# Optimization experiments

Measured on AMD Instinct MI355X. Metric: run time of the kernel, lower is better.

Reference implementation:

```python
import jax, jax.numpy as jnp
import numpy as np


def setup_inputs() -> dict:
    key = jax.random.key(0)
    ks = jax.random.split(key, 8)
    B, L, D, H, Dh = 2, 2048, 1024, 16, 64
    scale = 1.0 / np.sqrt(D)
    return {
        "inputs_q": jax.random.normal(ks[0], (B, L, D), jnp.float32),
        "inputs_kv": jax.random.normal(ks[1], (B, L, D), jnp.float32),
        "mask_k": jax.random.uniform(ks[2], (B, L), jnp.float32),
        "Wq": jax.random.normal(ks[3], (D, H, Dh), jnp.float32) * scale,
        "bq": jnp.zeros((H, Dh), jnp.float32),
        "Wk": jax.random.normal(ks[4], (D, H, Dh), jnp.float32) * scale,
        "bk": jnp.zeros((H, Dh), jnp.float32),
        "Wv": jax.random.normal(ks[5], (D, H, Dh), jnp.float32) * scale,
        "bv": jnp.zeros((H, Dh), jnp.float32),
        "Wo": jax.random.normal(ks[6], (H, Dh, D), jnp.float32) * (1.0 / np.sqrt(D)),
        "bo": jnp.zeros((D,), jnp.float32),
    }


def reference(inputs_q, inputs_kv, mask_k, Wq, bq, Wk, bk, Wv, bv, Wo, bo):
    # QKV projections: [B,L,D] x [D,H,Dh] -> [B,L,H,Dh]
    q = jnp.einsum("bld,dhk->blhk", inputs_q, Wq) + bq
    k = jnp.einsum("bld,dhk->blhk", inputs_kv, Wk) + bk
    v = jnp.einsum("bld,dhk->blhk", inputs_kv, Wv) + bv
    # vector mask applied to values per key position
    v = mask_k[:, :, None, None] * v
    head_dim = q.shape[-1]
    q = q / jnp.sqrt(jnp.asarray(head_dim, q.dtype))
    # attention scores [B,H,Lq,Lk]
    scores = jnp.einsum("bqhk,bshk->bhqs", q, k)
    probs = jax.nn.softmax(scores, axis=-1)
    # weighted values [B,Lq,H,Dh]
    x = jnp.einsum("bhqs,bshk->bqhk", probs, v)
    # output projection over (head, head_dim)
    out = jnp.einsum("bqhk,hkd->bqd", x, Wo) + bo
    return out
```

## Files before the change

### kernel.cpp

```cpp
#include <hip/hip_runtime.h>
#include <stdint.h>

typedef __attribute__((ext_vector_type(8))) short bf16x8;
typedef __attribute__((ext_vector_type(4))) float f32x4;
typedef __attribute__((ext_vector_type(16))) float f32x16;
typedef __attribute__((ext_vector_type(4))) unsigned short us4;
typedef __attribute__((ext_vector_type(4))) unsigned int u32x4;

#define AS1 __attribute__((address_space(1)))
#define AS3 __attribute__((address_space(3)))

static constexpr int Lq = 2048;
static constexpr int Dm = 1024;
static constexpr int NH = 16;
static constexpr int DH = 64;

__device__ __forceinline__ unsigned short f2bf(float x) {
  union { float f; uint32_t u; } v; v.f = x;
  uint32_t r = v.u + 0x7FFFu + ((v.u >> 16) & 1u);
  return (unsigned short)(r >> 16);
}

#if __has_builtin(__builtin_amdgcn_exp2f)
__device__ __forceinline__ float exp2_fast(float x) { return __builtin_amdgcn_exp2f(x); }
#else
__device__ __forceinline__ float exp2_fast(float x) {
  float r; asm volatile("v_exp_f32 %0, %1" : "=v"(r) : "v"(x)); return r;
}
#endif

__device__ __forceinline__ uint32_t cvtpk_bf16(float lo, float hi) {
  uint32_t r;
  asm("v_cvt_pk_bf16_f32 %0, %1, %2" : "=v"(r) : "v"(lo), "v"(hi));
  return r;
}

__device__ __forceinline__ f32x16 zero16() {
  f32x16 z;
#pragma unroll
  for (int i = 0; i < 16; ++i) z[i] = 0.f;
  return z;
}

__global__ __launch_bounds__(256) void cvt2_kernel(
    const float* __restrict__ s0, const float* __restrict__ s1,
    unsigned short* __restrict__ d0, unsigned short* __restrict__ d1, int n4) {
  const float* src = blockIdx.y ? s1 : s0;
  unsigned short* dst = blockIdx.y ? d1 : d0;
  int idx = blockIdx.x * 256 + threadIdx.x;
  int stride = gridDim.x * 256;
  for (int i = idx; i < n4; i += stride) {
    float4 f = ((const float4*)src)[i];
    us4 o = { f2bf(f.x), f2bf(f.y), f2bf(f.z), f2bf(f.w) };
    ((us4*)dst)[i] = o;
  }
}

__global__ __launch_bounds__(256) void tpose_kernel(
    const float* __restrict__ W0, const float* __restrict__ W1,
    const float* __restrict__ W2, const float* __restrict__ W3,
    unsigned short* __restrict__ T0, unsigned short* __restrict__ T1,
    unsigned short* __restrict__ T2, unsigned short* __restrict__ T3) {
  __shared__ float tile[32][33];
  const float* src; unsigned short* dst;
  switch (blockIdx.z) {
    case 0: src = W0; dst = T0; break;
    case 1: src = W1; dst = T1; break;
    case 2: src = W2; dst = T2; break;
    default: src = W3; dst = T3; break;
  }
  int x = threadIdx.x & 31, ys = threadIdx.x >> 5;
  int bx = blockIdx.x * 32, by = blockIdx.y * 32;
  for (int i = 0; i < 4; ++i) {
    int y = ys * 4 + i;
    tile[y][x] = src[(size_t)(by + y) * Dm + bx + x];
  }
  __syncthreads();
  for (int i = 0; i < 4; ++i) {
    int y = ys * 4 + i;
    dst[(size_t)(bx + y) * Dm + by + x] = f2bf(tile[x][y]);
  }
}

__global__ __launch_bounds__(512) void gemm_kernel(
    const unsigned short* __restrict__ A0, const unsigned short* __restrict__ A1,
    const unsigned short* __restrict__ W0, const unsigned short* __restrict__ W1,
    const unsigned short* __restrict__ W2,
    const float* __restrict__ b0, const float* __restrict__ b1,
    const float* __restrict__ b2, const float* __restrict__ mask,
    unsigned short* __restrict__ Qw, unsigned short* __restrict__ Kw,
    unsigned short* __restrict__ Vtw, float* __restrict__ Of, int modeBase) {
  const int mode = modeBase + blockIdx.z;
  const unsigned short* Ap = (mode == 1 || mode == 2) ? A1 : A0;
  const unsigned short* Wp = (mode == 1) ? W1 : ((mode == 2) ? W2 : W0);
  const float* bias = (mode == 1) ? b1 : ((mode == 2) ? b2 : b0);

  const int tid = threadIdx.x, lane = tid & 63, wid = tid >> 6;
  const int wm = wid >> 1, wn = wid & 1;
  const int m0 = blockIdx.x * 128, n0 = blockIdx.y * 128;
  const int ln = lane & 15, kg = lane >> 4;

  __shared__ __align__(16) unsigned short smem[24576];

  f32x4 acc[2][4];
#pragma unroll
  for (int i = 0; i < 2; ++i)
#pragma unroll
    for (int j = 0; j < 4; ++j) acc[i][j] = f32x4{0.f, 0.f, 0.f, 0.f};

  const int srow = tid >> 2;
  const int schx = (tid & 3) ^ ((srow >> 1) & 3);
  auto stage_g = [&](int buf, int k0) {
    __builtin_amdgcn_global_load_lds(
        (const AS1 unsigned int*)(Ap + (size_t)(m0 + srow) * Dm + k0 + schx * 8),
        (AS3 unsigned int*)&smem[buf * 4096 + wid * 512], 16, 0, 0);
    __builtin_amdgcn_global_load_lds(
        (const AS1 unsigned int*)(Wp + (size_t)(n0 + srow) * Dm + k0 + schx * 8),
        (AS3 unsigned int*)&smem[12288 + buf * 4096 + wid * 512], 16, 0, 0);
  };
  auto comp_g = [&](int buf) {
    const unsigned short* As = &smem[buf * 4096];
    const unsigned short* Bs = &smem[12288 + buf * 4096];
    const int rsw = kg ^ ((ln >> 1) & 3);
    bf16x8 af[2], bfv[4];
#pragma unroll
    for (int f = 0; f < 2; ++f)
      af[f] = *(const bf16x8*)&As[(wm * 32 + f * 16 + ln) * 32 + rsw * 8];
#pragma unroll
    for (int f = 0; f < 4; ++f)
      bfv[f] = *(const bf16x8*)&Bs[(wn * 64 + f * 16 + ln) * 32 + rsw * 8];
    __builtin_amdgcn_s_setprio(1);
#pragma unroll
    for (int mf = 0; mf < 2; ++mf)
#pragma unroll
      for (int nf = 0; nf < 4; ++nf)
        acc[mf][nf] = __builtin_amdgcn_mfma_f32_16x16x32_bf16(af[mf], bfv[nf],
                                                              acc[mf][nf], 0, 0, 0);
    __builtin_amdgcn_s_setprio(0);
  };

  stage_g(0, 0);
  stage_g(1, 32);
  for (int tt = 0; tt < 30; tt += 3) {
#pragma unroll
    for (int j = 0; j < 3; ++j) {
      const int t = tt + j;
      asm volatile("s_waitcnt vmcnt(2)" ::: "memory");
      asm volatile("s_barrier" ::: "memory");
      if (t < 30) stage_g((j + 2) % 3, (t + 2) * 32);
      comp_g(j);
    }
  }
  asm volatile("s_waitcnt vmcnt(2)" ::: "memory");
  asm volatile("s_barrier" ::: "memory");
  comp_g(0);
  asm volatile("s_waitcnt vmcnt(0)" ::: "memory");
  asm volatile("s_barrier" ::: "memory");
  comp_g(1);

  __syncthreads();
  unsigned short* ep = smem + wid * 2560;
  const int rowbase = m0 + wm * 32;
  const int colbase = n0 + wn * 64;

  if (mode <= 1) {
    unsigned short* dstbase = (mode == 0) ? Qw : Kw;
    const int hh = colbase >> 6;
    const int bb_ = rowbase >> 11, lb = rowbase & 2047;
    unsigned short* dst = dstbase + ((size_t)(bb_ * NH + hh) * Lq + lb) * DH;
    const float sc = (mode == 0) ? 0.18033688f : 1.0f;
    for (int nf = 0; nf < 4; ++nf) {
      const float bv_ = bias[colbase + nf * 16 + ln];
      for (int mf = 0; mf < 2; ++mf)
        for (int r = 0; r < 4; ++r)
          ep[(mf * 16 + kg * 4 + r) * 72 + nf * 16 + ln] =
              f2bf((acc[mf][nf][r] + bv_) * sc);
    }
    for (int it = 0; it < 4; ++it) {
      const int e = it * 64 + lane;
      const int rr = e >> 3, c = (e & 7) * 8;
      *(bf16x8*)(dst + (size_t)rr * DH + c) = *(const bf16x8*)&ep[rr * 72 + c];
    }
  } else if (mode == 2) {
    const int hh = colbase >> 6;
    const int bb_ = rowbase >> 11;
    const int l0 = rowbase & 2047;
    unsigned short* dst = Vtw + (size_t)(bb_ * NH + hh) * DH * Lq;
    for (int nf = 0; nf < 4; ++nf) {
      const int dh2 = nf * 16 + ln;
      const float bv_ = bias[colbase + dh2];
      for (int mf = 0; mf < 2; ++mf)
        for (int r = 0; r < 4; ++r) {
          const int rl = mf * 16 + kg * 4 + r;
          ep[dh2 * 40 + rl] = f2bf((acc[mf][nf][r] + bv_) * mask[rowbase + rl]);
        }
    }
    for (int it = 0; it < 4; ++it) {
      const int e = it * 64 + lane;
      const int dr = e >> 2, c = (e & 3) * 8;
      *(bf16x8*)(dst + (size_t)dr * Lq + l0 + c) = *(const bf16x8*)&ep[dr * 40 + c];
    }
  } else {
    float* epf = (float*)smem + wid * 1280;
    for (int mf = 0; mf < 2; ++mf) {
      for (int nf = 0; nf < 4; ++nf) {
        const float bv_ = bias[colbase + nf * 16 + ln];
        for (int r = 0; r < 4; ++r)
          epf[(kg * 4 + r) * 68 + nf * 16 + ln] = acc[mf][nf][r] + bv_;
      }
      for (int it = 0; it < 4; ++it) {
        const int e = it * 64 + lane;
        const int rr = e >> 4, c = (lane & 15) * 4;
        *(f32x4*)(Of + (size_t)(rowbase + mf * 16 + rr) * Dm + colbase + c) =
            *(const f32x4*)&epf[rr * 68 + c];
      }
    }
  }
}

__global__ __launch_bounds__(512) void attn_kernel(
    const unsigned short* __restrict__ Q, const unsigned short* __restrict__ K,
    const unsigned short* __restrict__ Vt, unsigned short* __restrict__ X) {
  const int tid = threadIdx.x, lane = tid & 63, wv = tid >> 6;
  const int lq = lane & 31, hi = lane >> 5;
  const int wq = wv & 3, half = wv >> 2;
  const int h = blockIdx.y, b = blockIdx.z;
  const int q0 = blockIdx.x * 128 + wq * 32;

  const size_t bh = (size_t)b * NH + h;
  const unsigned short* Qp = Q + bh * Lq * DH;
  const unsigned short* Kp = K + bh * Lq * DH + (size_t)half * 1024 * DH;
  const unsigned short* Vp = Vt + bh * DH * Lq + half * 1024;

  __shared__ __align__(16) unsigned short smem[24576];
  unsigned short* Klds = smem + half * 12288;
  unsigned short* Vlds = smem + half * 12288 + 6144;

  const int st = tid & 255;
  const int kr = st >> 3, kc = st & 7;
  const unsigned short* ksrc = Kp + (size_t)kr * DH + ((kc ^ (kr & 7)) * 8);
  const int vr = st >> 2, vc = st & 3;
  const unsigned short* vsrc = Vp + (size_t)vr * Lq + ((vc ^ ((vr >> 1) & 3)) * 8);

  auto stage = [&](int buf, const unsigned short* kp, const unsigned short* vp) {
    __builtin_amdgcn_global_load_lds((const AS1 unsigned int*)kp,
        (AS3 unsigned int*)&Klds[buf * 2048 + wq * 512], 16, 0, 0);
    __builtin_amdgcn_global_load_lds((const AS1 unsigned int*)vp,
        (AS3 unsigned int*)&Vlds[buf * 2048 + wq * 512], 16, 0, 0);
  };

  bf16x8 qf[4];
#pragma unroll
  for (int ks = 0; ks < 4; ++ks)
    qf[ks] = *(const bf16x8*)(Qp + (size_t)(q0 + lq) * DH + ks * 16 + hi * 8);

  bf16x8 onesf;
#pragma unroll
  for (int i = 0; i < 8; ++i) onesf[i] = (short)0x3F80;

  f32x16 o0 = zero16(), o1 = zero16(), lacc = zero16();

  auto compute = [&](const unsigned short* Kb, const unsigned short* Vb) {
    f32x16 s = zero16();
    __builtin_amdgcn_s_setprio(1);
#pragma unroll
    for (int ks = 0; ks < 4; ++ks) {
      const bf16x8 kfr =
          *(const bf16x8*)&Kb[lq * 64 + (((2 * ks + hi) ^ (lq & 7)) * 8)];
      s = __builtin_amdgcn_mfma_f32_32x32x16_bf16(kfr, qf[ks], s, 0, 0, 0);
    }
    __builtin_amdgcn_s_setprio(0);

    float p[16];
#pragma unroll
    for (int i = 0; i < 16; ++i) p[i] = exp2_fast(s[i]);

    uint32_t a00 = cvtpk_bf16(p[0],  p[1]),  a01 = cvtpk_bf16(p[2],  p[3]);
    uint32_t a10 = cvtpk_bf16(p[4],  p[5]),  a11 = cvtpk_bf16(p[6],  p[7]);
    uint32_t a20 = cvtpk_bf16(p[8],  p[9]),  a21 = cvtpk_bf16(p[10], p[11]);
    uint32_t a30 = cvtpk_bf16(p[12], p[13]), a31 = cvtpk_bf16(p[14], p[15]);
    asm volatile("v_permlane32_swap_b32 %0, %1" : "+v"(a00), "+v"(a10));
    asm volatile("v_permlane32_swap_b32 %0, %1" : "+v"(a01), "+v"(a11));
    asm volatile("v_permlane32_swap_b32 %0, %1" : "+v"(a20), "+v"(a30));
    asm volatile("v_permlane32_swap_b32 %0, %1" : "+v"(a21), "+v"(a31));
    u32x4 pw0 = {a00, a01, a10, a11};
    u32x4 pw1 = {a20, a21, a30, a31};
    const bf16x8 pa0 = *(const bf16x8*)&pw0;
    const bf16x8 pa1 = *(const bf16x8*)&pw1;

    __builtin_amdgcn_s_setprio(1);
    lacc = __builtin_amdgcn_mfma_f32_32x32x16_bf16(pa0, onesf, lacc, 0, 0, 0);
    lacc = __builtin_amdgcn_mfma_f32_32x32x16_bf16(pa1, onesf, lacc, 0, 0, 0);
    {
      const int sw0 = (lq >> 1) & 3;
      const bf16x8 vb0 = *(const bf16x8*)&Vb[lq * 32 + ((hi ^ sw0) * 8)];
      const bf16x8 vb1 = *(const bf16x8*)&Vb[lq * 32 + (((2 + hi) ^ sw0) * 8)];
      o0 = __builtin_amdgcn_mfma_f32_32x32x16_bf16(pa0, vb0, o0, 0, 0, 0);
      o0 = __builtin_amdgcn_mfma_f32_32x32x16_bf16(pa1, vb1, o0, 0, 0, 0);
      const int dh1 = 32 + lq;
      const int sw1 = (dh1 >> 1) & 3;
      const bf16x8 vb2 = *(const bf16x8*)&Vb[dh1 * 32 + ((hi ^ sw1) * 8)];
      const bf16x8 vb3 = *(const bf16x8*)&Vb[dh1 * 32 + (((2 + hi) ^ sw1) * 8)];
      o1 = __builtin_amdgcn_mfma_f32_32x32x16_bf16(pa0, vb2, o1, 0, 0, 0);
      o1 = __builtin_amdgcn_mfma_f32_32x32x16_bf16(pa1, vb3, o1, 0, 0, 0);
    }
    __builtin_amdgcn_s_setprio(0);
  };

  stage(0, ksrc, vsrc);
  stage(1, ksrc + 2048, vsrc + 32);
  const unsigned short* kpre = ksrc + 4096;
  const unsigned short* vpre = vsrc + 64;
  for (int tt = 0; tt < 30; tt += 3) {
#pragma unroll
    for (int j = 0; j < 3; ++j) {
      asm volatile("s_waitcnt vmcnt(2)" ::: "memory");
      asm volatile("s_barrier" ::: "memory");
      stage((j + 2) % 3, kpre, vpre);
      kpre += 2048; vpre += 32;
      compute(&Klds[j * 2048], &Vlds[j * 2048]);
    }
  }
  asm volatile("s_waitcnt vmcnt(2)" ::: "memory");
  asm volatile("s_barrier" ::: "memory");
  compute(&Klds[0], &Vlds[0]);
  asm volatile("s_waitcnt vmcnt(0)" ::: "memory");
  asm volatile("s_barrier" ::: "memory");
  compute(&Klds[2048], &Vlds[2048]);

  __syncthreads();
  float* cs = (float*)smem;
  float* po = cs + wq * 2048;
  float* pl = cs + 8192 + wq * 32;
  if (half == 1) {
#pragma unroll
    for (int r = 0; r < 16; ++r) {
      const int qrow = (r & 3) + 8 * (r >> 2) + 4 * hi;
      po[qrow * 64 + lq]      = o0[r];
      po[qrow * 64 + 32 + lq] = o1[r];
    }
    if (lq == 0) {
#pragma unroll
      for (int r = 0; r < 16; ++r)
        pl[(r & 3) + 8 * (r >> 2) + 4 * hi] = lacc[r];
    }
  }
  __syncthreads();
  if (half == 0) {
    unsigned short ou0[16], ou1[16];
#pragma unroll
    for (int r = 0; r < 16; ++r) {
      const int qrow = (r & 3) + 8 * (r >> 2) + 4 * hi;
      const float iv = 1.0f / (lacc[r] + pl[qrow]);
      ou0[r] = f2bf((o0[r] + po[qrow * 64 + lq]) * iv);
      ou1[r] = f2bf((o1[r] + po[qrow * 64 + 32 + lq]) * iv);
    }
    unsigned short* ep = (unsigned short*)po;
#pragma unroll
    for (int r = 0; r < 16; ++r) {
      const int qrow = (r & 3) + 8 * (r >> 2) + 4 * hi;
      ep[qrow * 72 + lq]      = ou0[r];
      ep[qrow * 72 + 32 + lq] = ou1[r];
    }
#pragma unroll
    for (int it = 0; it < 4; ++it) {
      const int e = it * 64 + lane;
      const int row = e >> 3, ch = e & 7;
      *(bf16x8*)(X + (size_t)(b * Lq + q0 + row) * Dm + h * DH + ch * 8) =
          *(const bf16x8*)&ep[row * 72 + ch * 8];
    }
  }
}

extern "C" void kernel_launch(void* const* d_in, const int* in_sizes, int n_in,
                              void* d_out, int out_size, void* d_ws, size_t ws_size,
                              hipStream_t stream) {
  (void)in_sizes; (void)n_in; (void)out_size; (void)ws_size;
  const float* inputs_q  = (const float*)d_in[0];
  const float* inputs_kv = (const float*)d_in[1];
  const float* mask_k    = (const float*)d_in[2];
  const float* Wq = (const float*)d_in[3];
  const float* bq = (const float*)d_in[4];
  const float* Wk = (const float*)d_in[5];
  const float* bk = (const float*)d_in[6];
  const float* Wv = (const float*)d_in[7];
  const float* bv = (const float*)d_in[8];
  const float* Wo = (const float*)d_in[9];
  const float* bo = (const float*)d_in[10];
  float* out = (float*)d_out;

  unsigned short* ws = (unsigned short*)d_ws;
  const size_t BIG = 4194304;
  const size_t WSZ = 1048576;
  unsigned short* Xq  = ws;
  unsigned short* Xkv = Xq + BIG;
  unsigned short* Wqt = Xkv + BIG;
  unsigned short* Wkt = Wqt + WSZ;
  unsigned short* Wvt = Wkt + WSZ;
  unsigned short* Wot = Wvt + WSZ;
  unsigned short* Qw  = Wot + WSZ;
  unsigned short* Kw  = Qw + BIG;
  unsigned short* Vtw = Kw + BIG;
  unsigned short* Xat = Vtw + BIG;

  cvt2_kernel<<<dim3(512, 2), 256, 0, stream>>>(inputs_q, inputs_kv, Xq, Xkv,
                                                (int)(BIG / 4));
  tpose_kernel<<<dim3(32, 32, 4), 256, 0, stream>>>(Wq, Wk, Wv, Wo, Wqt, Wkt, Wvt, Wot);
  gemm_kernel<<<dim3(32, 8, 3), 512, 0, stream>>>(Xq, Xkv, Wqt, Wkt, Wvt, bq, bk, bv,
                                                  mask_k, Qw, Kw, Vtw, nullptr, 0);
  attn_kernel<<<dim3(16, 16, 2), 512, 0, stream>>>(Qw, Kw, Vtw, Xat);
  gemm_kernel<<<dim3(32, 8, 1), 512, 0, stream>>>(Xat, nullptr, Wot, nullptr, nullptr,
                                                  bo, nullptr, nullptr, nullptr,
                                                  nullptr, nullptr, nullptr, out, 3);
}
```

Baseline: 104.6 us.

## Split attention keys across four wave groups with double-buffered LDS and XCD-aware block mapping

The attention kernel grows from 512 to 1024 threads per block, so four wave groups each process a quarter of the key sequence instead of two halves. The key loop changes from a three-buffer prefetch ring to a two-buffer scheme with an extra barrier after each compute step. Partial outputs are reduced serially through LDS in three rounds. A flattened 1D grid remaps block IDs so that blocks of the same batch and head land on the same XCD for L2 reuse. The aim is more split-K parallelism and better cache locality, at the cost of more barriers, less prefetch depth and a longer reduction epilogue.

```diff
diff --git a/kernel.cpp b/kernel.cpp
--- a/kernel.cpp
+++ b/kernel.cpp
@@ -218,23 +218,27 @@
   }
 }
 
-__global__ __launch_bounds__(512) void attn_kernel(
+__global__ __launch_bounds__(1024) void attn_kernel(
     const unsigned short* __restrict__ Q, const unsigned short* __restrict__ K,
     const unsigned short* __restrict__ Vt, unsigned short* __restrict__ X) {
   const int tid = threadIdx.x, lane = tid & 63, wv = tid >> 6;
   const int lq = lane & 31, hi = lane >> 5;
-  const int wq = wv & 3, half = wv >> 2;
-  const int h = blockIdx.y, b = blockIdx.z;
-  const int q0 = blockIdx.x * 128 + wq * 32;
+  const int wq = wv & 3, qu = wv >> 2;
+  const int bid = blockIdx.x;
+  const int slot = bid >> 3;
+  const int g = (bid & 7) * 4 + (slot >> 4);
+  const int qt = slot & 15;
+  const int h = g & 15, b = g >> 4;
+  const int q0 = qt * 128 + wq * 32;
 
   const size_t bh = (size_t)b * NH + h;
   const unsigned short* Qp = Q + bh * Lq * DH;
-  const unsigned short* Kp = K + bh * Lq * DH + (size_t)half * 1024 * DH;
-  const unsigned short* Vp = Vt + bh * DH * Lq + half * 1024;
-
-  __shared__ __align__(16) unsigned short smem[24576];
-  unsigned short* Klds = smem + half * 12288;
-  unsigned short* Vlds = smem + half * 12288 + 6144;
+  const unsigned short* Kp = K + bh * Lq * DH + (size_t)qu * 512 * DH;
+  const unsigned short* Vp = Vt + bh * DH * Lq + qu * 512;
+
+  __shared__ __align__(16) unsigned short smem[32768];
+  unsigned short* Klds = smem + qu * 8192;
+  unsigned short* Vlds = smem + qu * 8192 + 4096;
 
   const int st = tid & 255;
   const int kr = st >> 3, kc = st & 7;
@@ -260,7 +264,9 @@
 
   f32x16 o0 = zero16(), o1 = zero16(), lacc = zero16();
 
-  auto compute = [&](const unsigned short* Kb, const unsigned short* Vb) {
+  auto compute = [&](int buf) {
+    const unsigned short* Kb = &Klds[buf * 2048];
+    const unsigned short* Vb = &Vlds[buf * 2048];
     f32x16 s = zero16();
     __builtin_amdgcn_s_setprio(1);
 #pragma unroll
@@ -311,56 +317,63 @@
   stage(1, ksrc + 2048, vsrc + 32);
   const unsigned short* kpre = ksrc + 4096;
   const unsigned short* vpre = vsrc + 64;
-  for (int tt = 0; tt < 30; tt += 3) {
-#pragma unroll
-    for (int j = 0; j < 3; ++j) {
-      asm volatile("s_waitcnt vmcnt(2)" ::: "memory");
-      asm volatile("s_barrier" ::: "memory");
-      stage((j + 2) % 3, kpre, vpre);
-      kpre += 2048; vpre += 32;
-      compute(&Klds[j * 2048], &Vlds[j * 2048]);
-    }
+#pragma unroll 2
+  for (int t = 0; t < 14; ++t) {
+    asm volatile("s_waitcnt vmcnt(2)" ::: "memory");
+    asm volatile("s_barrier" ::: "memory");
+    compute(t & 1);
+    asm volatile("s_waitcnt lgkmcnt(0)" ::: "memory");
+    asm volatile("s_barrier" ::: "memory");
+    stage(t & 1, kpre, vpre);
+    kpre += 2048; vpre += 32;
   }
   asm volatile("s_waitcnt vmcnt(2)" ::: "memory");
   asm volatile("s_barrier" ::: "memory");
-  compute(&Klds[0], &Vlds[0]);
+  compute(0);
   asm volatile("s_waitcnt vmcnt(0)" ::: "memory");
   asm volatile("s_barrier" ::: "memory");
-  compute(&Klds[2048], &Vlds[2048]);
+  compute(1);
 
   __syncthreads();
   float* cs = (float*)smem;
   float* po = cs + wq * 2048;
   float* pl = cs + 8192 + wq * 32;
-  if (half == 1) {
+#pragma unroll
+  for (int rr = 1; rr < 4; ++rr) {
+    if (qu == rr) {
+#pragma unroll
+      for (int r = 0; r < 16; ++r) {
+        const int qrow = (r & 3) + 8 * (r >> 2) + 4 * hi;
+        po[qrow * 64 + lq]      = o0[r];
+        po[qrow * 64 + 32 + lq] = o1[r];
+      }
+      if (lq == 0) {
+#pragma unroll
+        for (int r = 0; r < 16; ++r)
+          pl[(r & 3) + 8 * (r >> 2) + 4 * hi] = lacc[r];
+      }
+    }
+    __syncthreads();
+    if (qu == 0) {
+#pragma unroll
+      for (int r = 0; r < 16; ++r) {
+        const int qrow = (r & 3) + 8 * (r >> 2) + 4 * hi;
+        o0[r]   += po[qrow * 64 + lq];
+        o1[r]   += po[qrow * 64 + 32 + lq];
+        lacc[r] += pl[qrow];
+      }
+    }
+    __syncthreads();
+  }
+
+  if (qu == 0) {
+    unsigned short* ep = (unsigned short*)po;
 #pragma unroll
     for (int r = 0; r < 16; ++r) {
       const int qrow = (r & 3) + 8 * (r >> 2) + 4 * hi;
-      po[qrow * 64 + lq]      = o0[r];
-      po[qrow * 64 + 32 + lq] = o1[r];
-    }
-    if (lq == 0) {
-#pragma unroll
-      for (int r = 0; r < 16; ++r)
-        pl[(r & 3) + 8 * (r >> 2) + 4 * hi] = lacc[r];
-    }
-  }
-  __syncthreads();
-  if (half == 0) {
-    unsigned short ou0[16], ou1[16];
-#pragma unroll
-    for (int r = 0; r < 16; ++r) {
-      const int qrow = (r & 3) + 8 * (r >> 2) + 4 * hi;
-      const float iv = 1.0f / (lacc[r] + pl[qrow]);
-      ou0[r] = f2bf((o0[r] + po[qrow * 64 + lq]) * iv);
-      ou1[r] = f2bf((o1[r] + po[qrow * 64 + 32 + lq]) * iv);
-    }
-    unsigned short* ep = (unsigned short*)po;
-#pragma unroll
-    for (int r = 0; r < 16; ++r) {
-      const int qrow = (r & 3) + 8 * (r >> 2) + 4 * hi;
-      ep[qrow * 72 + lq]      = ou0[r];
-      ep[qrow * 72 + 32 + lq] = ou1[r];
+      const float iv = 1.0f / lacc[r];
+      ep[qrow * 72 + lq]      = f2bf(o0[r] * iv);
+      ep[qrow * 72 + 32 + lq] = f2bf(o1[r] * iv);
     }
 #pragma unroll
     for (int it = 0; it < 4; ++it) {
@@ -408,7 +421,7 @@
   tpose_kernel<<<dim3(32, 32, 4), 256, 0, stream>>>(Wq, Wk, Wv, Wo, Wqt, Wkt, Wvt, Wot);
   gemm_kernel<<<dim3(32, 8, 3), 512, 0, stream>>>(Xq, Xkv, Wqt, Wkt, Wvt, bq, bk, bv,
                                                   mask_k, Qw, Kw, Vtw, nullptr, 0);
-  attn_kernel<<<dim3(16, 16, 2), 512, 0, stream>>>(Qw, Kw, Vtw, Xat);
+  attn_kernel<<<dim3(512, 1, 1), 1024, 0, stream>>>(Qw, Kw, Vtw, Xat);
   gemm_kernel<<<dim3(32, 8, 1), 512, 0, stream>>>(Xat, nullptr, Wot, nullptr, nullptr,
                                                   bo, nullptr, nullptr, nullptr,
                                                   nullptr, nullptr, nullptr, out, 3);
```

Measured after the change: 108.1 us. 1.03x slower.

## Give each attention wave two 32-row query tiles and remap blocks across XCDs

Applied to the files above, without the earlier changes.

The attention kernel drops from 8 waves to 4 per block. Each wave now handles 64 query rows as two 32-row MFMA tiles, so every K/V fragment read from LDS feeds twice as many MFMAs. Each thread issues four global-to-LDS loads per stage instead of two, with the vmcnt waits adjusted to match. The launch grid becomes 1D with a block-index remap that groups (batch, head) pairs per XCD for L2 locality, at the cost of roughly doubled accumulator registers per wave.

```diff
diff --git a/kernel.cpp b/kernel.cpp
--- a/kernel.cpp
+++ b/kernel.cpp
@@ -218,14 +218,18 @@
   }
 }
 
-__global__ __launch_bounds__(512) void attn_kernel(
+__global__ __launch_bounds__(256) void attn_kernel(
     const unsigned short* __restrict__ Q, const unsigned short* __restrict__ K,
     const unsigned short* __restrict__ Vt, unsigned short* __restrict__ X) {
   const int tid = threadIdx.x, lane = tid & 63, wv = tid >> 6;
   const int lq = lane & 31, hi = lane >> 5;
-  const int wq = wv & 3, half = wv >> 2;
-  const int h = blockIdx.y, b = blockIdx.z;
-  const int q0 = blockIdx.x * 128 + wq * 32;
+  const int qw = wv & 1, half = wv >> 1;
+  const int bid = blockIdx.x;
+  const int slot = bid >> 3;
+  const int g = (bid & 7) * 4 + (slot >> 4);
+  const int qt = slot & 15;
+  const int h = g & 15, b = g >> 4;
+  const int q0 = qt * 128 + qw * 64;
 
   const size_t bh = (size_t)b * NH + h;
   const unsigned short* Qp = Q + bh * Lq * DH;
@@ -236,134 +240,166 @@
   unsigned short* Klds = smem + half * 12288;
   unsigned short* Vlds = smem + half * 12288 + 6144;
 
-  const int st = tid & 255;
-  const int kr = st >> 3, kc = st & 7;
-  const unsigned short* ksrc = Kp + (size_t)kr * DH + ((kc ^ (kr & 7)) * 8);
-  const int vr = st >> 2, vc = st & 3;
-  const unsigned short* vsrc = Vp + (size_t)vr * Lq + ((vc ^ ((vr >> 1) & 3)) * 8);
-
-  auto stage = [&](int buf, const unsigned short* kp, const unsigned short* vp) {
-    __builtin_amdgcn_global_load_lds((const AS1 unsigned int*)kp,
-        (AS3 unsigned int*)&Klds[buf * 2048 + wq * 512], 16, 0, 0);
-    __builtin_amdgcn_global_load_lds((const AS1 unsigned int*)vp,
-        (AS3 unsigned int*)&Vlds[buf * 2048 + wq * 512], 16, 0, 0);
+  const int kcA = qw * 64 + lane;
+  const int krow = kcA >> 3, kch = kcA & 7;
+  const unsigned short* ksrcA = Kp + (size_t)krow * DH + ((kch ^ (krow & 7)) * 8);
+  const int vrow = kcA >> 2, vch = kcA & 3;
+  const unsigned short* vsrcA = Vp + (size_t)vrow * Lq + ((vch ^ ((vrow >> 1) & 3)) * 8);
+
+  auto stage = [&](int buf, int koff, int voff) {
+    __builtin_amdgcn_global_load_lds((const AS1 unsigned int*)(ksrcA + koff),
+        (AS3 unsigned int*)&Klds[buf * 2048 + qw * 512], 16, 0, 0);
+    __builtin_amdgcn_global_load_lds((const AS1 unsigned int*)(ksrcA + 1024 + koff),
+        (AS3 unsigned int*)&Klds[buf * 2048 + 1024 + qw * 512], 16, 0, 0);
+    __builtin_amdgcn_global_load_lds((const AS1 unsigned int*)(vsrcA + voff),
+        (AS3 unsigned int*)&Vlds[buf * 2048 + qw * 512], 16, 0, 0);
+    __builtin_amdgcn_global_load_lds((const AS1 unsigned int*)(vsrcA + 32 * Lq + voff),
+        (AS3 unsigned int*)&Vlds[buf * 2048 + 1024 + qw * 512], 16, 0, 0);
   };
 
-  bf16x8 qf[4];
-#pragma unroll
-  for (int ks = 0; ks < 4; ++ks)
-    qf[ks] = *(const bf16x8*)(Qp + (size_t)(q0 + lq) * DH + ks * 16 + hi * 8);
+  bf16x8 qfA[4], qfB[4];
+#pragma unroll
+  for (int ks = 0; ks < 4; ++ks) {
+    qfA[ks] = *(const bf16x8*)(Qp + (size_t)(q0 + lq) * DH + ks * 16 + hi * 8);
+    qfB[ks] = *(const bf16x8*)(Qp + (size_t)(q0 + 32 + lq) * DH + ks * 16 + hi * 8);
+  }
 
   bf16x8 onesf;
 #pragma unroll
   for (int i = 0; i < 8; ++i) onesf[i] = (short)0x3F80;
 
-  f32x16 o0 = zero16(), o1 = zero16(), lacc = zero16();
-
-  auto compute = [&](const unsigned short* Kb, const unsigned short* Vb) {
-    f32x16 s = zero16();
+  f32x16 o0A = zero16(), o1A = zero16(), lA = zero16();
+  f32x16 o0B = zero16(), o1B = zero16(), lB = zero16();
+
+  auto compute = [&](int buf) {
+    const unsigned short* Kb = &Klds[buf * 2048];
+    const unsigned short* Vb = &Vlds[buf * 2048];
+    f32x16 sA = zero16(), sB = zero16();
     __builtin_amdgcn_s_setprio(1);
 #pragma unroll
     for (int ks = 0; ks < 4; ++ks) {
       const bf16x8 kfr =
           *(const bf16x8*)&Kb[lq * 64 + (((2 * ks + hi) ^ (lq & 7)) * 8)];
-      s = __builtin_amdgcn_mfma_f32_32x32x16_bf16(kfr, qf[ks], s, 0, 0, 0);
+      sA = __builtin_amdgcn_mfma_f32_32x32x16_bf16(kfr, qfA[ks], sA, 0, 0, 0);
+      sB = __builtin_amdgcn_mfma_f32_32x32x16_bf16(kfr, qfB[ks], sB, 0, 0, 0);
     }
     __builtin_amdgcn_s_setprio(0);
 
-    float p[16];
-#pragma unroll
-    for (int i = 0; i < 16; ++i) p[i] = exp2_fast(s[i]);
-
-    uint32_t a00 = cvtpk_bf16(p[0],  p[1]),  a01 = cvtpk_bf16(p[2],  p[3]);
-    uint32_t a10 = cvtpk_bf16(p[4],  p[5]),  a11 = cvtpk_bf16(p[6],  p[7]);
-    uint32_t a20 = cvtpk_bf16(p[8],  p[9]),  a21 = cvtpk_bf16(p[10], p[11]);
-    uint32_t a30 = cvtpk_bf16(p[12], p[13]), a31 = cvtpk_bf16(p[14], p[15]);
+    float pA[16], pB[16];
+#pragma unroll
+    for (int i = 0; i < 16; ++i) { pA[i] = exp2_fast(sA[i]); pB[i] = exp2_fast(sB[i]); }
+
+    uint32_t a00 = cvtpk_bf16(pA[0],  pA[1]),  a01 = cvtpk_bf16(pA[2],  pA[3]);
+    uint32_t a10 = cvtpk_bf16(pA[4],  pA[5]),  a11 = cvtpk_bf16(pA[6],  pA[7]);
+    uint32_t a20 = cvtpk_bf16(pA[8],  pA[9]),  a21 = cvtpk_bf16(pA[10], pA[11]);
+    uint32_t a30 = cvtpk_bf16(pA[12], pA[13]), a31 = cvtpk_bf16(pA[14], pA[15]);
     asm volatile("v_permlane32_swap_b32 %0, %1" : "+v"(a00), "+v"(a10));
     asm volatile("v_permlane32_swap_b32 %0, %1" : "+v"(a01), "+v"(a11));
     asm volatile("v_permlane32_swap_b32 %0, %1" : "+v"(a20), "+v"(a30));
     asm volatile("v_permlane32_swap_b32 %0, %1" : "+v"(a21), "+v"(a31));
-    u32x4 pw0 = {a00, a01, a10, a11};
-    u32x4 pw1 = {a20, a21, a30, a31};
-    const bf16x8 pa0 = *(const bf16x8*)&pw0;
-    const bf16x8 pa1 = *(const bf16x8*)&pw1;
+    uint32_t b00 = cvtpk_bf16(pB[0],  pB[1]),  b01 = cvtpk_bf16(pB[2],  pB[3]);
+    uint32_t b10 = cvtpk_bf16(pB[4],  pB[5]),  b11 = cvtpk_bf16(pB[6],  pB[7]);
+    uint32_t b20 = cvtpk_bf16(pB[8],  pB[9]),  b21 = cvtpk_bf16(pB[10], pB[11]);
+    uint32_t b30 = cvtpk_bf16(pB[12], pB[13]), b31 = cvtpk_bf16(pB[14], pB[15]);
+    asm volatile("v_permlane32_swap_b32 %0, %1" : "+v"(b00), "+v"(b10));
+    asm volatile("v_permlane32_swap_b32 %0, %1" : "+v"(b01), "+v"(b11));
+    asm volatile("v_permlane32_swap_b32 %0, %1" : "+v"(b20), "+v"(b30));
+    asm volatile("v_permlane32_swap_b32 %0, %1" : "+v"(b21), "+v"(b31));
+    u32x4 pwA0 = {a00, a01, a10, a11}, pwA1 = {a20, a21, a30, a31};
+    u32x4 pwB0 = {b00, b01, b10, b11}, pwB1 = {b20, b21, b30, b31};
+    const bf16x8 paA0 = *(const bf16x8*)&pwA0, paA1 = *(const bf16x8*)&pwA1;
+    const bf16x8 paB0 = *(const bf16x8*)&pwB0, paB1 = *(const bf16x8*)&pwB1;
 
     __builtin_amdgcn_s_setprio(1);
-    lacc = __builtin_amdgcn_mfma_f32_32x32x16_bf16(pa0, onesf, lacc, 0, 0, 0);
-    lacc = __builtin_amdgcn_mfma_f32_32x32x16_bf16(pa1, onesf, lacc, 0, 0, 0);
+    lA = __builtin_amdgcn_mfma_f32_32x32x16_bf16(paA0, onesf, lA, 0, 0, 0);
+    lA = __builtin_amdgcn_mfma_f32_32x32x16_bf16(paA1, onesf, lA, 0, 0, 0);
+    lB = __builtin_amdgcn_mfma_f32_32x32x16_bf16(paB0, onesf, lB, 0, 0, 0);
+    lB = __builtin_amdgcn_mfma_f32_32x32x16_bf16(paB1, onesf, lB, 0, 0, 0);
     {
       const int sw0 = (lq >> 1) & 3;
       const bf16x8 vb0 = *(const bf16x8*)&Vb[lq * 32 + ((hi ^ sw0) * 8)];
       const bf16x8 vb1 = *(const bf16x8*)&Vb[lq * 32 + (((2 + hi) ^ sw0) * 8)];
-      o0 = __builtin_amdgcn_mfma_f32_32x32x16_bf16(pa0, vb0, o0, 0, 0, 0);
-      o0 = __builtin_amdgcn_mfma_f32_32x32x16_bf16(pa1, vb1, o0, 0, 0, 0);
+      o0A = __builtin_amdgcn_mfma_f32_32x32x16_bf16(paA0, vb0, o0A, 0, 0, 0);
+      o0A = __builtin_amdgcn_mfma_f32_32x32x16_bf16(paA1, vb1, o0A, 0, 0, 0);
+      o0B = __builtin_amdgcn_mfma_f32_32x32x16_bf16(paB0, vb0, o0B, 0, 0, 0);
+      o0B = __builtin_amdgcn_mfma_f32_32x32x16_bf16(paB1, vb1, o0B, 0, 0, 0);
       const int dh1 = 32 + lq;
       const int sw1 = (dh1 >> 1) & 3;
       const bf16x8 vb2 = *(const bf16x8*)&Vb[dh1 * 32 + ((hi ^ sw1) * 8)];
       const bf16x8 vb3 = *(const bf16x8*)&Vb[dh1 * 32 + (((2 + hi) ^ sw1) * 8)];
-      o1 = __builtin_amdgcn_mfma_f32_32x32x16_bf16(pa0, vb2, o1, 0, 0, 0);
-      o1 = __builtin_amdgcn_mfma_f32_32x32x16_bf16(pa1, vb3, o1, 0, 0, 0);
+      o1A = __builtin_amdgcn_mfma_f32_32x32x16_bf16(paA0, vb2, o1A, 0, 0, 0);
+      o1A = __builtin_amdgcn_mfma_f32_32x32x16_bf16(paA1, vb3, o1A, 0, 0, 0);
+      o1B = __builtin_amdgcn_mfma_f32_32x32x16_bf16(paB0, vb2, o1B, 0, 0, 0);
+      o1B = __builtin_amdgcn_mfma_f32_32x32x16_bf16(paB1, vb3, o1B, 0, 0, 0);
     }
     __builtin_amdgcn_s_setprio(0);
   };
 
-  stage(0, ksrc, vsrc);
-  stage(1, ksrc + 2048, vsrc + 32);
-  const unsigned short* kpre = ksrc + 4096;
-  const unsigned short* vpre = vsrc + 64;
+  stage(0, 0, 0);
+  stage(1, 2048, 32);
   for (int tt = 0; tt < 30; tt += 3) {
 #pragma unroll
     for (int j = 0; j < 3; ++j) {
-      asm volatile("s_waitcnt vmcnt(2)" ::: "memory");
+      const int t = tt + j;
+      asm volatile("s_waitcnt vmcnt(4)" ::: "memory");
       asm volatile("s_barrier" ::: "memory");
-      stage((j + 2) % 3, kpre, vpre);
-      kpre += 2048; vpre += 32;
-      compute(&Klds[j * 2048], &Vlds[j * 2048]);
-    }
-  }
-  asm volatile("s_waitcnt vmcnt(2)" ::: "memory");
+      stage((j + 2) % 3, (t + 2) * 2048, (t + 2) * 32);
+      compute(j);
+    }
+  }
+  asm volatile("s_waitcnt vmcnt(4)" ::: "memory");
   asm volatile("s_barrier" ::: "memory");
-  compute(&Klds[0], &Vlds[0]);
+  compute(0);
   asm volatile("s_waitcnt vmcnt(0)" ::: "memory");
   asm volatile("s_barrier" ::: "memory");
-  compute(&Klds[2048], &Vlds[2048]);
+  compute(1);
 
   __syncthreads();
   float* cs = (float*)smem;
-  float* po = cs + wq * 2048;
-  float* pl = cs + 8192 + wq * 32;
+  float* po = cs + qw * 4096;
+  float* pl = cs + 8192 + qw * 64;
   if (half == 1) {
 #pragma unroll
     for (int r = 0; r < 16; ++r) {
-      const int qrow = (r & 3) + 8 * (r >> 2) + 4 * hi;
-      po[qrow * 64 + lq]      = o0[r];
-      po[qrow * 64 + 32 + lq] = o1[r];
+      const int qr = (r & 3) + 8 * (r >> 2) + 4 * hi;
+      po[qr * 64 + lq]             = o0A[r];
+      po[qr * 64 + 32 + lq]        = o1A[r];
+      po[(qr + 32) * 64 + lq]      = o0B[r];
+      po[(qr + 32) * 64 + 32 + lq] = o1B[r];
     }
     if (lq == 0) {
 #pragma unroll
-      for (int r = 0; r < 16; ++r)
-        pl[(r & 3) + 8 * (r >> 2) + 4 * hi] = lacc[r];
+      for (int r = 0; r < 16; ++r) {
+        const int qr = (r & 3) + 8 * (r >> 2) + 4 * hi;
+        pl[qr]      = lA[r];
+        pl[qr + 32] = lB[r];
+      }
     }
   }
   __syncthreads();
   if (half == 0) {
-    unsigned short ou0[16], ou1[16];
+    unsigned short ou0A[16], ou1A[16], ou0B[16], ou1B[16];
 #pragma unroll
     for (int r = 0; r < 16; ++r) {
-      const int qrow = (r & 3) + 8 * (r >> 2) + 4 * hi;
-      const float iv = 1.0f / (lacc[r] + pl[qrow]);
-      ou0[r] = f2bf((o0[r] + po[qrow * 64 + lq]) * iv);
-      ou1[r] = f2bf((o1[r] + po[qrow * 64 + 32 + lq]) * iv);
+      const int qr = (r & 3) + 8 * (r >> 2) + 4 * hi;
+      const float ivA = 1.0f / (lA[r] + pl[qr]);
+      const float ivB = 1.0f / (lB[r] + pl[qr + 32]);
+      ou0A[r] = f2bf((o0A[r] + po[qr * 64 + lq]) * ivA);
+      ou1A[r] = f2bf((o1A[r] + po[qr * 64 + 32 + lq]) * ivA);
+      ou0B[r] = f2bf((o0B[r] + po[(qr + 32) * 64 + lq]) * ivB);
+      ou1B[r] = f2bf((o1B[r] + po[(qr + 32) * 64 + 32 + lq]) * ivB);
     }
     unsigned short* ep = (unsigned short*)po;
 #pragma unroll
     for (int r = 0; r < 16; ++r) {
-      const int qrow = (r & 3) + 8 * (r >> 2) + 4 * hi;
-      ep[qrow * 72 + lq]      = ou0[r];
-      ep[qrow * 72 + 32 + lq] = ou1[r];
-    }
-#pragma unroll
-    for (int it = 0; it < 4; ++it) {
+      const int qr = (r & 3) + 8 * (r >> 2) + 4 * hi;
+      ep[qr * 72 + lq]             = ou0A[r];
+      ep[qr * 72 + 32 + lq]        = ou1A[r];
+      ep[(qr + 32) * 72 + lq]      = ou0B[r];
+      ep[(qr + 32) * 72 + 32 + lq] = ou1B[r];
+    }
+#pragma unroll
+    for (int it = 0; it < 8; ++it) {
       const int e = it * 64 + lane;
       const int row = e >> 3, ch = e & 7;
       *(bf16x8*)(X + (size_t)(b * Lq + q0 + row) * Dm + h * DH + ch * 8) =
@@ -408,7 +444,7 @@
   tpose_kernel<<<dim3(32, 32, 4), 256, 0, stream>>>(Wq, Wk, Wv, Wo, Wqt, Wkt, Wvt, Wot);
   gemm_kernel<<<dim3(32, 8, 3), 512, 0, stream>>>(Xq, Xkv, Wqt, Wkt, Wvt, bq, bk, bv,
                                                   mask_k, Qw, Kw, Vtw, nullptr, 0);
-  attn_kernel<<<dim3(16, 16, 2), 512, 0, stream>>>(Qw, Kw, Vtw, Xat);
+  attn_kernel<<<dim3(512, 1, 1), 256, 0, stream>>>(Qw, Kw, Vtw, Xat);
   gemm_kernel<<<dim3(32, 8, 1), 512, 0, stream>>>(Xat, nullptr, Wot, nullptr, nullptr,
                                                   bo, nullptr, nullptr, nullptr,
                                                   nullptr, nullptr, nullptr, out, 3);
```

Result: slower. 116.6 us, median of 3 (+11.5%).
